# Kernel tuning notes

Hardware: AMD Instinct MI355X
Metric: run time of the kernel (lower is better)

## Reference

```python
import jax, jax.numpy as jnp
import numpy as np

N_SHOTS, N_SAMPLES, IMG = 10, 192, 256
M = N_SHOTS * N_SAMPLES  # 1920 k-space samples


def _radial_traj():
    # mri-nufft initialize_2D_radial: uniform spoke angles over pi,
    # radii in [-0.5, 0.5) with N_SAMPLES points per spoke.
    r = (np.arange(N_SAMPLES) - N_SAMPLES / 2) / N_SAMPLES
    ang = np.pi * np.arange(N_SHOTS) / N_SHOTS
    kx = np.cos(ang)[:, None] * r[None, :]
    ky = np.sin(ang)[:, None] * r[None, :]
    return np.stack([kx, ky], axis=-1).reshape(-1, 2).astype(np.float32)


def _phase_mats(samples):
    # Separable NDFT phase factors: exp(-2i*pi*k_x*i), exp(-2i*pi*k_y*j)
    grid = jnp.arange(IMG, dtype=jnp.float32) - IMG / 2  # centered pixel coords
    Ax = jnp.exp(-2j * jnp.pi * samples[:, 0:1] * grid[None, :]).astype(jnp.complex64)  # (M, IMG)
    Ay = jnp.exp(-2j * jnp.pi * samples[:, 1:2] * grid[None, :]).astype(jnp.complex64)  # (M, IMG)
    return Ax, Ay


def _pipe_density(samples, n_iter=10):
    # Pipe & Menon density compensation: w <- w / |F F^H w| (density=True in gpunufft).
    Ax, Ay = _phase_mats(samples)
    w = jnp.ones(M, jnp.complex64)
    for _ in range(n_iter):
        t = Ax.conj() * w[:, None]                    # (M, IMG)
        img = jnp.einsum('mi,mj->ij', t, Ay.conj())   # F^H w, (IMG, IMG)
        back = jnp.einsum('mi,ij,mj->m', Ax, img, Ay) # F F^H w, (M,)
        w = w / jnp.maximum(jnp.abs(back), 1e-12).astype(jnp.complex64)
    return jnp.abs(w).astype(jnp.float32)


def setup_inputs() -> dict:
    key = jax.random.key(0)
    k1, k2 = jax.random.split(key)
    B, C = 64, 1
    x_real = jax.random.normal(k1, (B, C, IMG, IMG), dtype=jnp.float32)
    x_imag = jax.random.normal(k2, (B, C, IMG, IMG), dtype=jnp.float32)
    samples = jnp.asarray(_radial_traj())
    density = _pipe_density(samples)
    return {"x_real": x_real, "x_imag": x_imag, "samples": samples, "density": density}


def reference(x_real, x_imag, samples, density):
    x = (x_real + 1j * x_imag).astype(jnp.complex64)  # (B, C, IMG, IMG)
    Ax, Ay = _phase_mats(samples)
    # Forward NUFFT (type-2 NDFT): kspace[b,c,m] = sum_ij Ax[m,i] Ay[m,j] x[b,c,i,j]
    t = jnp.einsum('mi,bcij->bcmj', Ax, x)            # (B, C, M, IMG)
    kspace = jnp.einsum('mj,bcmj->bcm', Ay, t)        # (B, C, M)
    # Density-compensated adjoint NUFFT (type-1 NDFT)
    kw = kspace * density.astype(jnp.complex64)
    u = jnp.einsum('mi,bcm->bcmi', Ax.conj(), kw)     # (B, C, M, IMG)
    adj = jnp.einsum('mj,bcmi->bcij', Ay.conj(), u) / (IMG * IMG)
    return jnp.stack([adj.real, adj.imag], axis=-1)   # (B, C, IMG, IMG, 2)
```

## Files before the change

### kernel.cpp

```cpp
#include <hip/hip_runtime.h>
#include <hip/hip_bf16.h>
#include <hip/hip_fp16.h>

constexpr int IMG_ = 256;
constexpr int M_   = 1920;
constexpr int B_   = 64;
constexpr int MI_  = M_ * IMG_;
constexpr int IMG2 = IMG_ * IMG_;

typedef _Float16 half8 __attribute__((ext_vector_type(8)));
typedef float    floatx4 __attribute__((ext_vector_type(4)));

__device__ __forceinline__ void gll16(const _Float16* g, _Float16* l) {
  __builtin_amdgcn_global_load_lds(
      (const __attribute__((address_space(1))) void*)g,
      (__attribute__((address_space(3))) void*)l, 16, 0, 0);
}

constexpr int PH1_N = MI_ / 256;
constexpr int PH2_N = 8 * IMG_;
constexpr int XT_N  = 8 * 8 * B_;

__global__ __launch_bounds__(256) void prep_k(
    const float* __restrict__ samples,
    const float* __restrict__ xr, const float* __restrict__ xi,
    _Float16* __restrict__ axh_r, _Float16* __restrict__ axh_i,
    _Float16* __restrict__ axtc_r, _Float16* __restrict__ axtc_i,
    _Float16* __restrict__ aytc_r, _Float16* __restrict__ aytc_i,
    _Float16* __restrict__ xth_r, _Float16* __restrict__ xth_i) {
  __shared__ float tr[32][33], ti[32][33];
  const int t = threadIdx.x;
  const int n = blockIdx.x;

  if (n < PH1_N) {
    int idx = n * 256 + t;
    int m = idx >> 8;
    int i = idx & 255;
    float g  = (float)i - 128.0f;
    float kx = samples[2 * m + 0];
    float sx, cx;
    sincospif(-2.0f * kx * g, &sx, &cx);
    axh_r[idx] = (_Float16)cx; axh_i[idx] = (_Float16)sx;
  } else if (n < PH1_N + PH2_N) {
    int nn = n - PH1_N;
    int m = (nn & 7) * 256 + t;
    int i = nn >> 3;
    if (m < M_) {
      float g  = (float)i - 128.0f;
      float kx = samples[2 * m + 0];
      float ky = samples[2 * m + 1];
      float sx, cx, sy, cy;
      sincospif(-2.0f * kx * g, &sx, &cx);
      sincospif(-2.0f * ky * g, &sy, &cy);
      int o = i * M_ + m;
      axtc_r[o] = (_Float16)cx; axtc_i[o] = (_Float16)(-sx);
      aytc_r[o] = (_Float16)cy; aytc_i[o] = (_Float16)(-sy);
    }
  } else {
    int nn = n - PH1_N - PH2_N;
    const int b  = nn >> 6;
    const int i0 = (nn & 7) * 32, j0 = ((nn >> 3) & 7) * 32;
    const int r = t >> 5, c = t & 31;
#pragma unroll
    for (int k = 0; k < 4; ++k) {
      int row = r + k * 8;
      tr[row][c] = xr[(size_t)b * IMG2 + (i0 + row) * IMG_ + j0 + c];
      ti[row][c] = xi[(size_t)b * IMG2 + (i0 + row) * IMG_ + j0 + c];
    }
    __syncthreads();
#pragma unroll
    for (int k = 0; k < 4; ++k) {
      int row = r + k * 8;
      xth_r[(size_t)b * IMG2 + (j0 + row) * IMG_ + i0 + c] = (_Float16)tr[c][row];
      xth_i[(size_t)b * IMG2 + (j0 + row) * IMG_ + i0 + c] = (_Float16)ti[c][row];
    }
  }
}


__global__ __launch_bounds__(256, 3) void fwd_k(
    const _Float16* __restrict__ axh_r, const _Float16* __restrict__ axh_i,
    const _Float16* __restrict__ aytc_r, const _Float16* __restrict__ aytc_i,
    const _Float16* __restrict__ xth_r, const _Float16* __restrict__ xth_i,
    float2* __restrict__ kpart) {
  __shared__ _Float16 lds[2][12288];

  const int t  = threadIdx.x;
  const int w  = t >> 6;
  const int l  = t & 63;
  const int lr = l & 15;
  const int q  = l >> 4;

  const int n     = blockIdx.x;
  const int r     = n >> 3;
  const int b     = (n & 7) + 8 * (r / 60);
  const int inner = r % 60;
  const int m0    = (inner % 30) * 64;
  const int jc    = inner / 30;
  const int j0    = jc * 128;

  const int srow   = l >> 2;
  const int schunk = (l & 3) ^ ((l >> 3) & 3);
  const int gA     = srow * IMG_ + schunk * 8;
  const int rc     = (q ^ ((lr >> 1) & 3)) << 3;

  const floatx4 z4 = {0.f, 0.f, 0.f, 0.f};
  floatx4 accr[4][2], acci[4][2];
#pragma unroll
  for (int mt = 0; mt < 4; ++mt)
#pragma unroll
    for (int jt = 0; jt < 2; ++jt) { accr[mt][jt] = z4; acci[mt][jt] = z4; }

  auto stage = [&](int buf, int s) {
    const int col = s * 32;
    _Float16* L = lds[buf];
    const size_t offA = (size_t)(m0 + w * 16) * IMG_ + col + gA;
    gll16(axh_r + offA, L + 0    + w * 512);
    gll16(axh_i + offA, L + 2048 + w * 512);
    const size_t offB = (size_t)b * IMG2 + (size_t)(j0 + w * 32) * IMG_ + col + gA;
    gll16(xth_r + offB,             L + 4096 + w * 1024);
    gll16(xth_r + offB + 16 * IMG_, L + 4096 + w * 1024 + 512);
    gll16(xth_i + offB,             L + 8192 + w * 1024);
    gll16(xth_i + offB + 16 * IMG_, L + 8192 + w * 1024 + 512);
  };

  auto compute = [&](int buf) {
    const _Float16* L = lds[buf];
    half8 br[2], bi[2], nbi[2];
#pragma unroll
    for (int jt = 0; jt < 2; ++jt) {
      const int ro = (w * 32 + jt * 16 + lr) * 32 + rc;
      br[jt]  = *(const half8*)&L[4096 + ro];
      bi[jt]  = *(const half8*)&L[8192 + ro];
      nbi[jt] = -bi[jt];
    }
#pragma unroll
    for (int mt = 0; mt < 4; ++mt) {
      const int ro = (mt * 16 + lr) * 32 + rc;
      half8 ar = *(const half8*)&L[0 + ro];
      half8 ai = *(const half8*)&L[2048 + ro];
#pragma unroll
      for (int jt = 0; jt < 2; ++jt) {
        accr[mt][jt] = __builtin_amdgcn_mfma_f32_16x16x32_f16(ar, br[jt],  accr[mt][jt], 0, 0, 0);
        accr[mt][jt] = __builtin_amdgcn_mfma_f32_16x16x32_f16(ai, nbi[jt], accr[mt][jt], 0, 0, 0);
        acci[mt][jt] = __builtin_amdgcn_mfma_f32_16x16x32_f16(ar, bi[jt],  acci[mt][jt], 0, 0, 0);
        acci[mt][jt] = __builtin_amdgcn_mfma_f32_16x16x32_f16(ai, br[jt],  acci[mt][jt], 0, 0, 0);
      }
    }
  };

  stage(0, 0);
  __syncthreads();
#pragma unroll
  for (int s = 0; s < 8; ++s) {
    const int buf = s & 1;
    if (s < 7) stage(buf ^ 1, s + 1);
    compute(buf);
    __syncthreads();
  }

  float kr[4][4] = {}, ki[4][4] = {};
#pragma unroll
  for (int mt = 0; mt < 4; ++mt) {
    const int mb = m0 + mt * 16 + q * 4;
#pragma unroll
    for (int jt = 0; jt < 2; ++jt) {
      const int j = j0 + w * 32 + jt * 16 + lr;
      const __half2* yr2 = (const __half2*)&aytc_r[(size_t)j * M_ + mb];
      const __half2* yi2 = (const __half2*)&aytc_i[(size_t)j * M_ + mb];
      const __half2 yr01 = yr2[0], yr23 = yr2[1];
      const __half2 yi01 = yi2[0], yi23 = yi2[1];
      const float yrv[4] = {__low2float(yr01), __high2float(yr01),
                            __low2float(yr23), __high2float(yr23)};
      const float yiv[4] = {-__low2float(yi01), -__high2float(yi01),
                            -__low2float(yi23), -__high2float(yi23)};
#pragma unroll
      for (int reg = 0; reg < 4; ++reg) {
        const float tr = accr[mt][jt][reg], ti = acci[mt][jt][reg];
        kr[mt][reg] = fmaf(yrv[reg], tr, fmaf(-yiv[reg], ti, kr[mt][reg]));
        ki[mt][reg] = fmaf(yrv[reg], ti, fmaf(yiv[reg], tr, ki[mt][reg]));
      }
    }
  }

#pragma unroll
  for (int mt = 0; mt < 4; ++mt)
#pragma unroll
    for (int reg = 0; reg < 4; ++reg)
#pragma unroll
      for (int off = 1; off < 16; off <<= 1) {
        kr[mt][reg] += __shfl_xor(kr[mt][reg], off);
        ki[mt][reg] += __shfl_xor(ki[mt][reg], off);
      }

  float2* scr = (float2*)&lds[0][0];
  if (lr == 0) {
#pragma unroll
    for (int mt = 0; mt < 4; ++mt)
#pragma unroll
      for (int reg = 0; reg < 4; ++reg)
        scr[w * 64 + mt * 16 + q * 4 + reg] = make_float2(kr[mt][reg], ki[mt][reg]);
  }
  __syncthreads();
  if (t < 64) {
    float sr = 0.f, si = 0.f;
#pragma unroll
    for (int ww = 0; ww < 4; ++ww) {
      const float2 p = scr[ww * 64 + t];
      sr += p.x; si += p.y;
    }
    kpart[((size_t)jc * B_ + b) * M_ + m0 + t] = make_float2(sr, si);
  }
}

__global__ __launch_bounds__(256) void comb_k(
    const float2* __restrict__ kpart, const float* __restrict__ density,
    _Float16* __restrict__ kwh_r, _Float16* __restrict__ kwh_i) {
  const int idx = blockIdx.x * 256 + threadIdx.x;
  if (idx >= B_ * M_) return;
  const int m = idx % M_;
  const float2 p0 = kpart[idx];
  const float2 p1 = kpart[(size_t)B_ * M_ + idx];
  const float d = density[m];
  kwh_r[idx] = (_Float16)((p0.x + p1.x) * d);
  kwh_i[idx] = (_Float16)((p0.y + p1.y) * d);
}

__global__ __launch_bounds__(256, 3) void adj_k(
    const _Float16* __restrict__ axtc_r, const _Float16* __restrict__ axtc_i,
    const _Float16* __restrict__ aytc_r, const _Float16* __restrict__ aytc_i,
    const _Float16* __restrict__ kwh_r, const _Float16* __restrict__ kwh_i,
    float* __restrict__ out) {
  __shared__ _Float16 lds[2][12288];

  const int t  = threadIdx.x;
  const int w  = t >> 6;
  const int l  = t & 63;
  const int lr = l & 15;
  const int q  = l >> 4;
  const int b  = blockIdx.z;
  const int i0 = blockIdx.x * 64;
  const int j0 = blockIdx.y * 128;

  const int srow   = l >> 2;
  const int schunk = (l & 3) ^ ((l >> 3) & 3);
  const int gA     = srow * M_ + schunk * 8;
  const int rc     = (q ^ ((lr >> 1) & 3)) << 3;

  const int wrow = t >> 1;
  const int wh   = t & 1;
  const int wp   = (wrow >> 1) & 3;
  const int wc0  = ((2 * wh + 0) ^ wp) << 3;
  const int wc1  = ((2 * wh + 1) ^ wp) << 3;

  const floatx4 z4 = {0.f, 0.f, 0.f, 0.f};
  floatx4 accr[4][2], acci[4][2];
#pragma unroll
  for (int mt = 0; mt < 4; ++mt)
#pragma unroll
    for (int jt = 0; jt < 2; ++jt) { accr[mt][jt] = z4; acci[mt][jt] = z4; }

  uint4 Yr0, Yr1, Yi0, Yi1, Cr0, Cr1, Ci0, Ci1;

  auto stageA = [&](int buf, int s) {
    const int mc = s * 32;
    _Float16* L = lds[buf];
    const size_t off = (size_t)(i0 + w * 16) * M_ + mc + gA;
    gll16(axtc_r + off, L + 0    + w * 512);
    gll16(axtc_i + off, L + 2048 + w * 512);
  };

  auto loadW = [&](int s) {
    const int mc = s * 32 + wh * 16;
    const size_t oy = (size_t)(j0 + wrow) * M_ + mc;
    const size_t oc = (size_t)b * M_ + mc;
    Yr0 = *(const uint4*)&aytc_r[oy];  Yr1 = *(const uint4*)&aytc_r[oy + 8];
    Yi0 = *(const uint4*)&aytc_i[oy];  Yi1 = *(const uint4*)&aytc_i[oy + 8];
    Cr0 = *(const uint4*)&kwh_r[oc];   Cr1 = *(const uint4*)&kwh_r[oc + 8];
    Ci0 = *(const uint4*)&kwh_i[oc];   Ci1 = *(const uint4*)&kwh_i[oc + 8];
  };

  auto writeW = [&](int buf) {
    __half2 Wr0[4], Wi0[4], Wr1[4], Wi1[4];
    {
      const __half2* yr = (const __half2*)&Yr0; const __half2* yi = (const __half2*)&Yi0;
      const __half2* cr = (const __half2*)&Cr0; const __half2* ci = (const __half2*)&Ci0;
#pragma unroll
      for (int e = 0; e < 4; ++e) {
        Wr0[e] = __hsub2(__hmul2(cr[e], yr[e]), __hmul2(ci[e], yi[e]));
        Wi0[e] = __hfma2(cr[e], yi[e], __hmul2(ci[e], yr[e]));
      }
    }
    {
      const __half2* yr = (const __half2*)&Yr1; const __half2* yi = (const __half2*)&Yi1;
      const __half2* cr = (const __half2*)&Cr1; const __half2* ci = (const __half2*)&Ci1;
#pragma unroll
      for (int e = 0; e < 4; ++e) {
        Wr1[e] = __hsub2(__hmul2(cr[e], yr[e]), __hmul2(ci[e], yi[e]));
        Wi1[e] = __hfma2(cr[e], yi[e], __hmul2(ci[e], yr[e]));
      }
    }
    _Float16* Lr = lds[buf] + 4096;
    _Float16* Li = lds[buf] + 8192;
    const int rb = wrow * 32;
    *(uint4*)&Lr[rb + wc0] = *(const uint4*)&Wr0[0];
    *(uint4*)&Lr[rb + wc1] = *(const uint4*)&Wr1[0];
    *(uint4*)&Li[rb + wc0] = *(const uint4*)&Wi0[0];
    *(uint4*)&Li[rb + wc1] = *(const uint4*)&Wi1[0];
  };

  auto compute = [&](int buf) {
    const _Float16* L = lds[buf];
    half8 br[2], bi[2], nbi[2];
#pragma unroll
    for (int jt = 0; jt < 2; ++jt) {
      const int ro = (w * 32 + jt * 16 + lr) * 32 + rc;
      br[jt]  = *(const half8*)&L[4096 + ro];
      bi[jt]  = *(const half8*)&L[8192 + ro];
      nbi[jt] = -bi[jt];
    }
#pragma unroll
    for (int mt = 0; mt < 4; ++mt) {
      const int ro = (mt * 16 + lr) * 32 + rc;
      half8 ar = *(const half8*)&L[0 + ro];
      half8 ai = *(const half8*)&L[2048 + ro];
#pragma unroll
      for (int jt = 0; jt < 2; ++jt) {
        accr[mt][jt] = __builtin_amdgcn_mfma_f32_16x16x32_f16(ar, br[jt],  accr[mt][jt], 0, 0, 0);
        accr[mt][jt] = __builtin_amdgcn_mfma_f32_16x16x32_f16(ai, nbi[jt], accr[mt][jt], 0, 0, 0);
        acci[mt][jt] = __builtin_amdgcn_mfma_f32_16x16x32_f16(ar, bi[jt],  acci[mt][jt], 0, 0, 0);
        acci[mt][jt] = __builtin_amdgcn_mfma_f32_16x16x32_f16(ai, br[jt],  acci[mt][jt], 0, 0, 0);
      }
    }
  };

  loadW(0);
  stageA(0, 0);
  writeW(0);
  __syncthreads();
#pragma unroll 2
  for (int s = 0; s < 60; ++s) {
    const int buf = s & 1;
    if (s < 59) { stageA(buf ^ 1, s + 1); loadW(s + 1); }
    compute(buf);
    if (s < 59) writeW(buf ^ 1);
    __syncthreads();
  }

  const float sc = 1.0f / (float)IMG2;
#pragma unroll
  for (int mt = 0; mt < 4; ++mt)
#pragma unroll
    for (int jt = 0; jt < 2; ++jt) {
      const int jg = j0 + w * 32 + jt * 16 + lr;
#pragma unroll
      for (int reg = 0; reg < 4; ++reg) {
        const int ig = i0 + mt * 16 + q * 4 + reg;
        float2 v = make_float2(accr[mt][jt][reg] * sc, acci[mt][jt][reg] * sc);
        *(float2*)&out[((size_t)(b * IMG_ + ig) * IMG_ + jg) * 2] = v;
      }
    }
}

extern "C" void kernel_launch(void* const* d_in, const int* in_sizes, int n_in,
                              void* d_out, int out_size, void* d_ws, size_t ws_size,
                              hipStream_t stream) {
  (void)in_sizes; (void)n_in; (void)out_size; (void)ws_size;

  const float* xr      = (const float*)d_in[0];
  const float* xi      = (const float*)d_in[1];
  const float* samples = (const float*)d_in[2];
  const float* density = (const float*)d_in[3];
  float* out = (float*)d_out;

  _Float16* f = (_Float16*)d_ws;
  _Float16* axh_r  = f + 0 * MI_;
  _Float16* axh_i  = f + 1 * MI_;
  _Float16* axtc_r = f + 4 * MI_;
  _Float16* axtc_i = f + 5 * MI_;
  _Float16* aytc_r = f + 6 * MI_;
  _Float16* aytc_i = f + 7 * MI_;
  _Float16* kwh_r  = f + 8 * MI_;
  _Float16* kwh_i  = kwh_r + B_ * M_;

  _Float16* xth_r = (_Float16*)d_out;
  _Float16* xth_i = xth_r + (size_t)B_ * IMG2;
  float2*   kpart = (float2*)(xth_i + (size_t)B_ * IMG2);

  prep_k<<<PH1_N + PH2_N + XT_N, 256, 0, stream>>>(
      samples, xr, xi, axh_r, axh_i,
      axtc_r, axtc_i, aytc_r, aytc_i, xth_r, xth_i);
  fwd_k<<<3840, 256, 0, stream>>>(axh_r, axh_i, aytc_r, aytc_i,
                                  xth_r, xth_i, kpart);
  comb_k<<<(B_ * M_ + 255) / 256, 256, 0, stream>>>(kpart, density, kwh_r, kwh_i);
  adj_k<<<dim3(4, 2, B_), 256, 0, stream>>>(axtc_r, axtc_i, aytc_r, aytc_i,
                                            kwh_r, kwh_i, out);
}
```

Measured before the change: 264.5 us.

## Fuse j-chunk reduction and density weighting into forward kernel, drop comb_k

Each forward block now loops over both 128-column j-chunks, running the Ay epilogue after each chunk and accumulating partial k-space sums in a dedicated shared scratch. It then applies the density weight and writes fp16 weighted k-space directly. This removes the separate combine kernel launch and the float2 partial-sum round trip through global memory. The cost is half as many blocks (1920), each with twice the serial work, which lowers parallelism and may cut latency hiding.

Result: slower. 270.2 us (+2.2%).

```diff
diff --git a/kernel.cpp b/kernel.cpp
--- a/kernel.cpp
+++ b/kernel.cpp
@@ -82,8 +82,10 @@
     const _Float16* __restrict__ axh_r, const _Float16* __restrict__ axh_i,
     const _Float16* __restrict__ aytc_r, const _Float16* __restrict__ aytc_i,
     const _Float16* __restrict__ xth_r, const _Float16* __restrict__ xth_i,
-    float2* __restrict__ kpart) {
+    const float* __restrict__ density,
+    _Float16* __restrict__ kwh_r, _Float16* __restrict__ kwh_i) {
   __shared__ _Float16 lds[2][12288];
+  __shared__ float2 scr[4][64];
 
   const int t  = threadIdx.x;
   const int w  = t >> 6;
@@ -91,13 +93,11 @@
   const int lr = l & 15;
   const int q  = l >> 4;
 
-  const int n     = blockIdx.x;
-  const int r     = n >> 3;
-  const int b     = (n & 7) + 8 * (r / 60);
-  const int inner = r % 60;
-  const int m0    = (inner % 30) * 64;
-  const int jc    = inner / 30;
-  const int j0    = jc * 128;
+  const int n   = blockIdx.x;
+  const int xcd = n & 7;
+  const int r   = n >> 3;
+  const int b   = xcd + 8 * (r / 30);
+  const int m0  = (r % 30) * 64;
 
   const int srow   = l >> 2;
   const int schunk = (l & 3) ^ ((l >> 3) & 3);
@@ -112,12 +112,13 @@
     for (int jt = 0; jt < 2; ++jt) { accr[mt][jt] = z4; acci[mt][jt] = z4; }
 
   auto stage = [&](int buf, int s) {
-    const int col = s * 32;
+    const int jc  = s >> 3;
+    const int col = (s & 7) * 32;
     _Float16* L = lds[buf];
     const size_t offA = (size_t)(m0 + w * 16) * IMG_ + col + gA;
     gll16(axh_r + offA, L + 0    + w * 512);
     gll16(axh_i + offA, L + 2048 + w * 512);
-    const size_t offB = (size_t)b * IMG2 + (size_t)(j0 + w * 32) * IMG_ + col + gA;
+    const size_t offB = (size_t)b * IMG2 + (size_t)(jc * 128 + w * 32) * IMG_ + col + gA;
     gll16(xth_r + offB,             L + 4096 + w * 1024);
     gll16(xth_r + offB + 16 * IMG_, L + 4096 + w * 1024 + 512);
     gll16(xth_i + offB,             L + 8192 + w * 1024);
@@ -149,81 +150,78 @@
     }
   };
 
+  auto epi = [&](int jc) {
+#pragma unroll
+    for (int mt = 0; mt < 4; ++mt) {
+      const int mb = m0 + mt * 16 + q * 4;
+      float kr[4] = {}, ki[4] = {};
+#pragma unroll
+      for (int jt = 0; jt < 2; ++jt) {
+        const int j = jc * 128 + w * 32 + jt * 16 + lr;
+        const __half2* yr2 = (const __half2*)&aytc_r[(size_t)j * M_ + mb];
+        const __half2* yi2 = (const __half2*)&aytc_i[(size_t)j * M_ + mb];
+        const __half2 yr01 = yr2[0], yr23 = yr2[1];
+        const __half2 yi01 = yi2[0], yi23 = yi2[1];
+        const float yrv[4] = {__low2float(yr01), __high2float(yr01),
+                              __low2float(yr23), __high2float(yr23)};
+        const float yiv[4] = {-__low2float(yi01), -__high2float(yi01),
+                              -__low2float(yi23), -__high2float(yi23)};
+#pragma unroll
+        for (int reg = 0; reg < 4; ++reg) {
+          const float tr = accr[mt][jt][reg], ti = acci[mt][jt][reg];
+          kr[reg] = fmaf(yrv[reg], tr, fmaf(-yiv[reg], ti, kr[reg]));
+          ki[reg] = fmaf(yrv[reg], ti, fmaf(yiv[reg], tr, ki[reg]));
+        }
+        accr[mt][jt] = z4;
+        acci[mt][jt] = z4;
+      }
+#pragma unroll
+      for (int reg = 0; reg < 4; ++reg)
+#pragma unroll
+        for (int off = 1; off < 16; off <<= 1) {
+          kr[reg] += __shfl_xor(kr[reg], off);
+          ki[reg] += __shfl_xor(ki[reg], off);
+        }
+      if (lr == 0) {
+#pragma unroll
+        for (int reg = 0; reg < 4; ++reg) {
+          const int ml = mt * 16 + q * 4 + reg;
+          if (jc == 0) {
+            scr[w][ml] = make_float2(kr[reg], ki[reg]);
+          } else {
+            float2 p = scr[w][ml];
+            scr[w][ml] = make_float2(p.x + kr[reg], p.y + ki[reg]);
+          }
+        }
+      }
+    }
+  };
+
   stage(0, 0);
   __syncthreads();
 #pragma unroll
-  for (int s = 0; s < 8; ++s) {
+  for (int s = 0; s < 16; ++s) {
     const int buf = s & 1;
-    if (s < 7) stage(buf ^ 1, s + 1);
+    if (s < 15) stage(buf ^ 1, s + 1);
     compute(buf);
+    if (s == 7) epi(0);
     __syncthreads();
   }
-
-  float kr[4][4] = {}, ki[4][4] = {};
-#pragma unroll
-  for (int mt = 0; mt < 4; ++mt) {
-    const int mb = m0 + mt * 16 + q * 4;
-#pragma unroll
-    for (int jt = 0; jt < 2; ++jt) {
-      const int j = j0 + w * 32 + jt * 16 + lr;
-      const __half2* yr2 = (const __half2*)&aytc_r[(size_t)j * M_ + mb];
-      const __half2* yi2 = (const __half2*)&aytc_i[(size_t)j * M_ + mb];
-      const __half2 yr01 = yr2[0], yr23 = yr2[1];
-      const __half2 yi01 = yi2[0], yi23 = yi2[1];
-      const float yrv[4] = {__low2float(yr01), __high2float(yr01),
-                            __low2float(yr23), __high2float(yr23)};
-      const float yiv[4] = {-__low2float(yi01), -__high2float(yi01),
-                            -__low2float(yi23), -__high2float(yi23)};
-#pragma unroll
-      for (int reg = 0; reg < 4; ++reg) {
-        const float tr = accr[mt][jt][reg], ti = acci[mt][jt][reg];
-        kr[mt][reg] = fmaf(yrv[reg], tr, fmaf(-yiv[reg], ti, kr[mt][reg]));
-        ki[mt][reg] = fmaf(yrv[reg], ti, fmaf(yiv[reg], tr, ki[mt][reg]));
-      }
-    }
-  }
-
-#pragma unroll
-  for (int mt = 0; mt < 4; ++mt)
-#pragma unroll
-    for (int reg = 0; reg < 4; ++reg)
-#pragma unroll
-      for (int off = 1; off < 16; off <<= 1) {
-        kr[mt][reg] += __shfl_xor(kr[mt][reg], off);
-        ki[mt][reg] += __shfl_xor(ki[mt][reg], off);
-      }
-
-  float2* scr = (float2*)&lds[0][0];
-  if (lr == 0) {
-#pragma unroll
-    for (int mt = 0; mt < 4; ++mt)
-#pragma unroll
-      for (int reg = 0; reg < 4; ++reg)
-        scr[w * 64 + mt * 16 + q * 4 + reg] = make_float2(kr[mt][reg], ki[mt][reg]);
-  }
+  epi(1);
   __syncthreads();
+
   if (t < 64) {
     float sr = 0.f, si = 0.f;
 #pragma unroll
     for (int ww = 0; ww < 4; ++ww) {
-      const float2 p = scr[ww * 64 + t];
+      const float2 p = scr[ww][t];
       sr += p.x; si += p.y;
     }
-    kpart[((size_t)jc * B_ + b) * M_ + m0 + t] = make_float2(sr, si);
+    const int m = m0 + t;
+    const float d = density[m];
+    kwh_r[b * M_ + m] = (_Float16)(sr * d);
+    kwh_i[b * M_ + m] = (_Float16)(si * d);
   }
-}
-
-__global__ __launch_bounds__(256) void comb_k(
-    const float2* __restrict__ kpart, const float* __restrict__ density,
-    _Float16* __restrict__ kwh_r, _Float16* __restrict__ kwh_i) {
-  const int idx = blockIdx.x * 256 + threadIdx.x;
-  if (idx >= B_ * M_) return;
-  const int m = idx % M_;
-  const float2 p0 = kpart[idx];
-  const float2 p1 = kpart[(size_t)B_ * M_ + idx];
-  const float d = density[m];
-  kwh_r[idx] = (_Float16)((p0.x + p1.x) * d);
-  kwh_i[idx] = (_Float16)((p0.y + p1.y) * d);
 }
 
 __global__ __launch_bounds__(256, 3) void adj_k(
@@ -385,14 +383,12 @@
 
   _Float16* xth_r = (_Float16*)d_out;
   _Float16* xth_i = xth_r + (size_t)B_ * IMG2;
-  float2*   kpart = (float2*)(xth_i + (size_t)B_ * IMG2);
 
   prep_k<<<PH1_N + PH2_N + XT_N, 256, 0, stream>>>(
       samples, xr, xi, axh_r, axh_i,
       axtc_r, axtc_i, aytc_r, aytc_i, xth_r, xth_i);
-  fwd_k<<<3840, 256, 0, stream>>>(axh_r, axh_i, aytc_r, aytc_i,
-                                  xth_r, xth_i, kpart);
-  comb_k<<<(B_ * M_ + 255) / 256, 256, 0, stream>>>(kpart, density, kwh_r, kwh_i);
+  fwd_k<<<1920, 256, 0, stream>>>(axh_r, axh_i, aytc_r, aytc_i,
+                                  xth_r, xth_i, density, kwh_r, kwh_i);
   adj_k<<<dim3(4, 2, B_), 256, 0, stream>>>(axtc_r, axtc_i, aytc_r, aytc_i,
                                             kwh_r, kwh_i, out);
 }
```
